# Performance work log

Hardware: AMD Instinct MI355X
Metric: run time of the kernel (lower is better)

Reference implementation:

```python
import jax, jax.numpy as jnp
import numpy as np

B, N, D, H = 2, 2048, 1024, 16
DH = D // H
SCALE = 1.0 / np.sqrt(DH).astype(np.float32)


def setup_inputs() -> dict:
    key = jax.random.key(0)
    k1, k2, k3, k4, k5 = jax.random.split(key, 5)
    x = jax.random.normal(k1, (B, N, D), dtype=jnp.float32)
    attn_bias = jax.random.normal(k2, (B, N, N), dtype=jnp.float32)
    # valid lengths in [N//2, N]; True = keep
    lengths = jax.random.randint(k3, (B,), N // 2, N + 1)
    key_padding_mask = jnp.arange(N)[None, :] < lengths[:, None]
    Wqkv = jax.random.normal(k4, (3 * D, D), dtype=jnp.float32) / np.sqrt(D)
    Wproj = jax.random.normal(k5, (D, D), dtype=jnp.float32) / np.sqrt(D)
    bproj = jnp.zeros((D,), dtype=jnp.float32)
    return {"x": x, "attn_bias": attn_bias, "key_padding_mask": key_padding_mask,
            "Wqkv": Wqkv, "Wproj": Wproj, "bproj": bproj}


def reference(x, attn_bias, key_padding_mask, Wqkv, Wproj, bproj):
    b, n, d = x.shape
    qkv = x @ Wqkv.T                                   # [B,N,3D]
    qkv = qkv.reshape(b, n, 3, H, DH)
    q = jnp.transpose(qkv[:, :, 0], (0, 2, 1, 3))      # [B,H,N,DH]
    k = jnp.transpose(qkv[:, :, 1], (0, 2, 1, 3))
    v = jnp.transpose(qkv[:, :, 2], (0, 2, 1, 3))
    attn = jnp.einsum('bhnd,bhmd->bhnm', q, k) * SCALE  # [B,H,N,N]
    attn = attn + attn_bias[:, None, :, :]
    attn = jnp.where(key_padding_mask[:, None, None, :], attn, -jnp.inf)
    attn = jax.nn.softmax(attn, axis=-1)
    y = jnp.einsum('bhnm,bhmd->bhnd', attn, v)          # [B,H,N,DH]
    y = jnp.transpose(y, (0, 2, 1, 3)).reshape(b, n, d)
    return y @ Wproj.T + bproj
```

## Files before the change

### kernel.cpp

```cpp
#include <hip/hip_runtime.h>
#include <hip/hip_bf16.h>

namespace {

typedef short short8 __attribute__((ext_vector_type(8)));
typedef float f32x4 __attribute__((ext_vector_type(4)));

#define L2E 1.4426950408889634f
#define SB() __builtin_amdgcn_sched_barrier(0)

__device__ __forceinline__ unsigned short f2bf(float f) {
  union { __hip_bfloat16 h; unsigned short u; } cv;
  cv.h = __float2bfloat16(f);
  return cv.u;
}

__device__ __forceinline__ unsigned cvt_pk_bf16(float lo, float hi) {
  unsigned r;
  asm("v_cvt_pk_bf16_f32 %0, %1, %2" : "=v"(r) : "v"(lo), "v"(hi));
  return r;
}

__device__ __forceinline__ void load_lds16(const void* g, void* l) {
  __builtin_amdgcn_global_load_lds((__attribute__((address_space(1))) void*)g,
                                   (__attribute__((address_space(3))) void*)l,
                                   16, 0, 0);
}

__device__ __forceinline__ int pi64(int rho) {
  const int c32 = rho & 32;
  const int o = (rho >> 4) & 1;
  const int g = (rho >> 2) & 3;
  const int s = rho & 3;
  return c32 + (o ? (((g ^ 2) << 3) + 4 + s) : ((g << 3) + s));
}

__global__ __launch_bounds__(256) void cvt_all(const float4* __restrict__ x,
                                               const float4* __restrict__ wqkv,
                                               const float4* __restrict__ wproj,
                                               const float4* __restrict__ biasf,
                                               ushort4* __restrict__ xb,
                                               ushort4* __restrict__ wqkvb,
                                               ushort4* __restrict__ wprojb,
                                               ushort4* __restrict__ bias16) {
  int i = blockIdx.x * 256 + threadIdx.x;
  if (i < 2097152) {
    const float4* src;
    ushort4* dst;
    int off;
    if (i < 1048576) { src = x; dst = xb; off = i; }
    else if (i < 1048576 + 786432) { src = wqkv; dst = wqkvb; off = i - 1048576; }
    else { src = wproj; dst = wprojb; off = i - (1048576 + 786432); }
    float4 f = src[off];
    ushort4 u;
    u.x = f2bf(f.x); u.y = f2bf(f.y); u.z = f2bf(f.z); u.w = f2bf(f.w);
    dst[off] = u;
  } else {
    const int off = i - 2097152;
    float4 f = biasf[off];
    ushort4 u;
    u.x = f2bf(f.x * L2E); u.y = f2bf(f.y * L2E);
    u.z = f2bf(f.z * L2E); u.w = f2bf(f.w * L2E);
    bias16[off] = u;
  }
}

__global__ __launch_bounds__(256) void gemm_qkv(const unsigned short* __restrict__ Xb,
                                                const unsigned short* __restrict__ Wb,
                                                unsigned short* __restrict__ qws,
                                                unsigned short* __restrict__ kws,
                                                unsigned short* __restrict__ vTws) {
  __shared__ unsigned short lA[128 * 32];
  __shared__ unsigned short lB[128 * 32];
  const int t = threadIdx.x;
  const int w = t >> 6, l = t & 63;
  const int wm = w >> 1, wn = w & 1;
  const int lr = l & 15, lg = l >> 4;
  const int row0 = blockIdx.x * 128, col0 = blockIdx.y * 128;
  const int srow = t >> 2;
  const int schunk = (t & 3) ^ (srow & 3);
  f32x4 acc[4][4] = {};
  for (int k0 = 0; k0 < 1024; k0 += 32) {
    __syncthreads();
    load_lds16(Xb + (size_t)(row0 + srow) * 1024 + k0 + schunk * 8, &lA[w * 512]);
    load_lds16(Xb + (size_t)(row0 + 64 + srow) * 1024 + k0 + schunk * 8, &lA[2048 + w * 512]);
    load_lds16(Wb + (size_t)(col0 + srow) * 1024 + k0 + schunk * 8, &lB[w * 512]);
    load_lds16(Wb + (size_t)(col0 + 64 + srow) * 1024 + k0 + schunk * 8, &lB[2048 + w * 512]);
    __syncthreads();
    short8 af[4], bf[4];
    const int rslot = (lg ^ (l & 3)) * 8;
#pragma unroll
    for (int mi = 0; mi < 4; ++mi)
      af[mi] = *(const short8*)&lA[(wm * 64 + mi * 16 + lr) * 32 + rslot];
#pragma unroll
    for (int ni = 0; ni < 4; ++ni)
      bf[ni] = *(const short8*)&lB[(wn * 64 + ni * 16 + lr) * 32 + rslot];
#pragma unroll
    for (int mi = 0; mi < 4; ++mi)
#pragma unroll
      for (int ni = 0; ni < 4; ++ni)
        acc[mi][ni] = __builtin_amdgcn_mfma_f32_16x16x32_bf16(af[mi], bf[ni], acc[mi][ni], 0, 0, 0);
  }
#pragma unroll
  for (int mi = 0; mi < 4; ++mi)
#pragma unroll
    for (int ni = 0; ni < 4; ++ni) {
      const int col = col0 + wn * 64 + ni * 16 + lr;
      const int s = col >> 10, rem = col & 1023;
      const int hh = rem >> 6, dh = rem & 63;
      const int row = row0 + wm * 64 + mi * 16 + lg * 4;
      const int bb = row >> 11, n = row & 2047;
      const size_t bh = (size_t)(bb * 16 + hh);
      if (s == 2) {
        ushort4 u4;
        u4.x = f2bf(acc[mi][ni][0]); u4.y = f2bf(acc[mi][ni][1]);
        u4.z = f2bf(acc[mi][ni][2]); u4.w = f2bf(acc[mi][ni][3]);
        *(ushort4*)&vTws[(bh * 64 + dh) * 2048 + n] = u4;
      } else if (s == 0) {
#pragma unroll
        for (int r = 0; r < 4; ++r)
          qws[(bh * 2048 + n + r) * 64 + dh] = f2bf(acc[mi][ni][r] * 0.18033688011112042f);
      } else {
#pragma unroll
        for (int r = 0; r < 4; ++r)
          kws[(bh * 2048 + n + r) * 64 + dh] = f2bf(acc[mi][ni][r]);
      }
    }
}

template <bool BB>
__global__ __launch_bounds__(256, 4) void attn_fwd(const unsigned short* __restrict__ qws,
                                                   const unsigned short* __restrict__ kws,
                                                   const unsigned short* __restrict__ vTws,
                                                   const float* __restrict__ bias,
                                                   const unsigned short* __restrict__ bias16,
                                                   const int* __restrict__ mask,
                                                   unsigned short* __restrict__ ctx) {
  __shared__ unsigned short lK[2][64 * 64];
  __shared__ unsigned short lVT[2][64 * 64];
  __shared__ int lred[4];
  const int t = threadIdx.x, w = t >> 6, l = t & 63;
  const int lr = l & 15, lg = l >> 4;
  const int xr7 = lr & 7;

  const int lin = blockIdx.x;
  const int xcd = lin & 7;
  const int r7 = lin >> 3;
  const int G = xcd * 8 + (r7 & 7);
  const int h = r7 >> 3;
  const int b = G & 1;
  const int qt = G >> 1;

  const size_t bh = (size_t)(b * 16 + h);
  const unsigned short* Q = qws + bh * (2048 * 64);
  const unsigned short* K = kws + bh * (2048 * 64);
  const unsigned short* VT = vTws + bh * (64 * 2048);

  const int* mrow = mask + b * 2048;
  int scnt = 0;
#pragma unroll
  for (int i = 0; i < 8; ++i) scnt += (mrow[t + i * 256] != 0);
#pragma unroll
  for (int d = 1; d < 64; d <<= 1) scnt += __shfl_xor(scnt, d, 64);
  if (l == 0) lred[w] = scnt;
  __syncthreads();
  const int len = lred[0] + lred[1] + lred[2] + lred[3];
  const int nt = ((((len + 63) >> 6) + 1) & ~1);

  const int qv = qt * 64 + w * 16 + lr;
  const short8 qf0 = *(const short8*)&Q[(size_t)qv * 64 + lg * 8];
  const short8 qf1 = *(const short8*)&Q[(size_t)qv * 64 + 32 + lg * 8];
  const float* bq = bias + (size_t)b * (2048 * 2048) + (size_t)qv * 2048;
  const unsigned short* bq16 = bias16 + (size_t)b * (2048 * 2048) + (size_t)qv * 2048;

  const int be = lg * 8, bo = ((lg ^ 2) * 8) + 4;
  const int boffs[4] = {be, bo, 32 + be, 32 + bo};

  short8 vones;
#pragma unroll
  for (int i = 0; i < 8; ++i) vones[i] = (short)0x3F80;

  f32x4 o[5] = {};

  const int sr = l >> 3;
  const int sc = ((l & 7) ^ sr) * 8;

  auto STAGE = [&](int ti2) {
    const int slot = ti2 & 1;
    const int kt2 = ti2 << 6;
#pragma unroll
    for (int u = 0; u < 2; ++u) {
      const int row = w * 16 + u * 8 + sr;
      load_lds16(K + (size_t)(kt2 + pi64(row)) * 64 + sc, &lK[slot][(w * 16 + u * 8) * 64]);
      load_lds16(VT + (size_t)row * 2048 + kt2 + sc, &lVT[slot][(w * 16 + u * 8) * 64]);
    }
  };
  auto LOADB = [&](auto& d, int ti2) {
    const int kt2 = ti2 << 6;
    if constexpr (BB) {
#pragma unroll
      for (int j = 0; j < 4; ++j) d[j] = *(const uint2*)&bq16[kt2 + boffs[j]];
    } else {
#pragma unroll
      for (int j = 0; j < 4; ++j) d[j] = *(const float4*)&bq[kt2 + boffs[j]];
    }
  };
  auto COMPUTE = [&](int ti, auto& b4, bool hn2) {
    const int slot = ti & 1;
    const int kt = ti << 6;
    const unsigned short* lKs = lK[slot];
    const unsigned short* lVs = lVT[slot];
    f32x4 s4[4];
    __builtin_amdgcn_s_setprio(1);
#pragma unroll
    for (int j = 0; j < 4; ++j) {
      f32x4 sj = {-16.f, -16.f, -16.f, -16.f};
      const int krow = (j * 16 + lr) * 64;
      short8 kf0 = *(const short8*)&lKs[krow + (lg ^ xr7) * 8];
      short8 kf1 = *(const short8*)&lKs[krow + ((lg + 4) ^ xr7) * 8];
      sj = __builtin_amdgcn_mfma_f32_16x16x32_bf16(kf0, qf0, sj, 0, 0, 0);
      sj = __builtin_amdgcn_mfma_f32_16x16x32_bf16(kf1, qf1, sj, 0, 0, 0);
      s4[j] = sj;
    }
    __builtin_amdgcn_s_setprio(0);
    if (kt + 64 <= len) {
#pragma unroll
      for (int j = 0; j < 4; ++j) {
        if constexpr (BB) {
          s4[j][0] += __uint_as_float(b4[j].x << 16);
          s4[j][1] += __uint_as_float(b4[j].x & 0xFFFF0000u);
          s4[j][2] += __uint_as_float(b4[j].y << 16);
          s4[j][3] += __uint_as_float(b4[j].y & 0xFFFF0000u);
        } else {
          s4[j][0] = fmaf(b4[j].x, L2E, s4[j][0]);
          s4[j][1] = fmaf(b4[j].y, L2E, s4[j][1]);
          s4[j][2] = fmaf(b4[j].z, L2E, s4[j][2]);
          s4[j][3] = fmaf(b4[j].w, L2E, s4[j][3]);
        }
      }
    } else {
#pragma unroll
      for (int j = 0; j < 4; ++j) {
        const int kb = kt + boffs[j];
        float bv[4];
        if constexpr (BB) {
          bv[0] = __uint_as_float(b4[j].x << 16);
          bv[1] = __uint_as_float(b4[j].x & 0xFFFF0000u);
          bv[2] = __uint_as_float(b4[j].y << 16);
          bv[3] = __uint_as_float(b4[j].y & 0xFFFF0000u);
#pragma unroll
          for (int r = 0; r < 4; ++r)
            s4[j][r] = (kb + r < len) ? (s4[j][r] + bv[r]) : -1e30f;
        } else {
          const float* bp = &b4[j].x;
#pragma unroll
          for (int r = 0; r < 4; ++r)
            s4[j][r] = (kb + r < len) ? fmaf(bp[r], L2E, s4[j][r]) : -1e30f;
        }
      }
    }
    if (hn2) LOADB(b4, ti + 2);
#pragma unroll
    for (int j = 0; j < 4; ++j)
#pragma unroll
      for (int r = 0; r < 4; ++r) s4[j][r] = __builtin_amdgcn_exp2f(s4[j][r]);
    unsigned wj0[4], wj1[4];
#pragma unroll
    for (int j = 0; j < 4; ++j) {
      wj0[j] = cvt_pk_bf16(s4[j][0], s4[j][1]);
      wj1[j] = cvt_pk_bf16(s4[j][2], s4[j][3]);
    }
#pragma unroll
    for (int c = 0; c < 2; ++c) {
      union { unsigned u[4]; short8 s8; } pu;
      pu.u[0] = wj0[2 * c];
      pu.u[1] = wj1[2 * c];
      pu.u[2] = (unsigned)__shfl_xor((int)wj0[2 * c + 1], 32, 64);
      pu.u[3] = (unsigned)__shfl_xor((int)wj1[2 * c + 1], 32, 64);
      __builtin_amdgcn_s_setprio(1);
#pragma unroll
      for (int ni = 0; ni < 4; ++ni) {
        short8 vf = *(const short8*)&lVs[(ni * 16 + lr) * 64 + ((c * 4 + lg) ^ xr7) * 8];
        o[ni] = __builtin_amdgcn_mfma_f32_16x16x32_bf16(pu.s8, vf, o[ni], 0, 0, 0);
      }
      o[4] = __builtin_amdgcn_mfma_f32_16x16x32_bf16(pu.s8, vones, o[4], 0, 0, 0);
      __builtin_amdgcn_s_setprio(0);
    }
  };

  float4 bA[4], bB[4];
  uint2 uA[4], uB[4];
  SB();
  STAGE(0);
  SB();
  if constexpr (BB) { LOADB(uA, 0); LOADB(uB, 1); }
  else              { LOADB(bA, 0); LOADB(bB, 1); }
  SB();
  asm volatile("s_waitcnt vmcnt(4)" ::: "memory");
  __builtin_amdgcn_s_barrier();
  SB();

  for (int ti = 0; ti < nt; ti += 2) {
    const bool h2 = (ti + 2 < nt);
    SB();
    STAGE(ti + 1);
    SB();
    if constexpr (BB) COMPUTE(ti, uA, h2); else COMPUTE(ti, bA, h2);
    SB();
    asm volatile("s_waitcnt vmcnt(4) lgkmcnt(0)" ::: "memory");
    __builtin_amdgcn_s_barrier();
    SB();
    if (h2) { STAGE(ti + 2); SB(); }
    if constexpr (BB) COMPUTE(ti + 1, uB, h2); else COMPUTE(ti + 1, bB, h2);
    if (h2) {
      SB();
      asm volatile("s_waitcnt vmcnt(4) lgkmcnt(0)" ::: "memory");
      __builtin_amdgcn_s_barrier();
      SB();
    }
  }

  float linv[4];
#pragma unroll
  for (int r = 0; r < 4; ++r) linv[r] = __builtin_amdgcn_rcpf(o[4][r]);
#pragma unroll
  for (int r = 0; r < 4; ++r) {
    const size_t orow = (size_t)b * 2048 + qt * 64 + w * 16 + lg * 4 + r;
#pragma unroll
    for (int ni = 0; ni < 4; ++ni)
      ctx[orow * 1024 + h * 64 + ni * 16 + lr] = f2bf(o[ni][r] * linv[r]);
  }
}

__global__ __launch_bounds__(256) void gemm_proj(const unsigned short* __restrict__ Cb,
                                                 const unsigned short* __restrict__ Wb,
                                                 const float* __restrict__ bproj,
                                                 float* __restrict__ out) {
  __shared__ unsigned short lA[128 * 32];
  __shared__ unsigned short lB[128 * 32];
  const int t = threadIdx.x;
  const int w = t >> 6, l = t & 63;
  const int wm = w >> 1, wn = w & 1;
  const int lr = l & 15, lg = l >> 4;
  const int row0 = blockIdx.x * 128, col0 = blockIdx.y * 128;
  const int srow = t >> 2;
  const int schunk = (t & 3) ^ (srow & 3);
  f32x4 acc[4][4] = {};
  for (int k0 = 0; k0 < 1024; k0 += 32) {
    __syncthreads();
    load_lds16(Cb + (size_t)(row0 + srow) * 1024 + k0 + schunk * 8, &lA[w * 512]);
    load_lds16(Cb + (size_t)(row0 + 64 + srow) * 1024 + k0 + schunk * 8, &lA[2048 + w * 512]);
    load_lds16(Wb + (size_t)(col0 + srow) * 1024 + k0 + schunk * 8, &lB[w * 512]);
    load_lds16(Wb + (size_t)(col0 + 64 + srow) * 1024 + k0 + schunk * 8, &lB[2048 + w * 512]);
    __syncthreads();
    short8 af[4], bf[4];
    const int rslot = (lg ^ (l & 3)) * 8;
#pragma unroll
    for (int mi = 0; mi < 4; ++mi)
      af[mi] = *(const short8*)&lA[(wm * 64 + mi * 16 + lr) * 32 + rslot];
#pragma unroll
    for (int ni = 0; ni < 4; ++ni)
      bf[ni] = *(const short8*)&lB[(wn * 64 + ni * 16 + lr) * 32 + rslot];
#pragma unroll
    for (int mi = 0; mi < 4; ++mi)
#pragma unroll
      for (int ni = 0; ni < 4; ++ni)
        acc[mi][ni] = __builtin_amdgcn_mfma_f32_16x16x32_bf16(af[mi], bf[ni], acc[mi][ni], 0, 0, 0);
  }
#pragma unroll
  for (int mi = 0; mi < 4; ++mi)
#pragma unroll
    for (int ni = 0; ni < 4; ++ni) {
      const int col = col0 + wn * 64 + ni * 16 + lr;
      const float bp = bproj[col];
#pragma unroll
      for (int r = 0; r < 4; ++r) {
        const int row = row0 + wm * 64 + mi * 16 + lg * 4 + r;
        out[(size_t)row * 1024 + col] = acc[mi][ni][r] + bp;
      }
    }
}

}

extern "C" void kernel_launch(void* const* d_in, const int* in_sizes, int n_in,
                              void* d_out, int out_size, void* d_ws, size_t ws_size,
                              hipStream_t stream) {
  (void)in_sizes; (void)n_in; (void)out_size;
  const float* x        = (const float*)d_in[0];
  const float* attnbias = (const float*)d_in[1];
  const int*   mask     = (const int*)d_in[2];
  const float* Wqkv     = (const float*)d_in[3];
  const float* Wproj    = (const float*)d_in[4];
  const float* bproj    = (const float*)d_in[5];
  float* out = (float*)d_out;

  unsigned short* ws     = (unsigned short*)d_ws;
  unsigned short* xb     = ws;
  unsigned short* wqkvb  = xb + 4194304;
  unsigned short* wprojb = wqkvb + 3145728;
  unsigned short* qws    = wprojb + 1048576;
  unsigned short* kws    = qws + 4194304;
  unsigned short* vTws   = kws + 4194304;
  unsigned short* ctxb   = vTws + 4194304;
  unsigned short* bias16 = ctxb + 4194304;

  const bool bb = ws_size >= (size_t)67108864;

  cvt_all<<<bb ? 16384 : 8192, 256, 0, stream>>>(
      (const float4*)x, (const float4*)Wqkv, (const float4*)Wproj,
      (const float4*)attnbias, (ushort4*)xb, (ushort4*)wqkvb, (ushort4*)wprojb,
      (ushort4*)bias16);
  gemm_qkv<<<dim3(32, 24), 256, 0, stream>>>(xb, wqkvb, qws, kws, vTws);
  if (bb)
    attn_fwd<true><<<1024, 256, 0, stream>>>(qws, kws, vTws, attnbias, bias16, mask, ctxb);
  else
    attn_fwd<false><<<1024, 256, 0, stream>>>(qws, kws, vTws, attnbias, bias16, mask, ctxb);
  gemm_proj<<<dim3(32, 8), 256, 0, stream>>>(ctxb, wprojb, bproj, out);
}
```

Baseline: 155.0 us.

## Overlap bias bf16 conversion with QKV GEMM and simplify mask length count

Moves the attention-bias fp32-to-bf16 conversion out of the standalone conversion kernel and into extra blocks of the QKV GEMM grid, so the memory-bound conversion runs alongside the compute-bound GEMM. In the attention kernel, each wave now counts the mask length on its own using int4 loads, which removes the shared-memory reduction and a block barrier. The trade-off is that the extra GEMM-grid blocks compete with GEMM tiles for compute units and bandwidth, and every wave repeats the mask reads.

```diff
diff --git a/kernel.cpp b/kernel.cpp
--- a/kernel.cpp
+++ b/kernel.cpp
@@ -38,41 +38,44 @@
 __global__ __launch_bounds__(256) void cvt_all(const float4* __restrict__ x,
                                                const float4* __restrict__ wqkv,
                                                const float4* __restrict__ wproj,
-                                               const float4* __restrict__ biasf,
                                                ushort4* __restrict__ xb,
                                                ushort4* __restrict__ wqkvb,
-                                               ushort4* __restrict__ wprojb,
-                                               ushort4* __restrict__ bias16) {
+                                               ushort4* __restrict__ wprojb) {
   int i = blockIdx.x * 256 + threadIdx.x;
-  if (i < 2097152) {
-    const float4* src;
-    ushort4* dst;
-    int off;
-    if (i < 1048576) { src = x; dst = xb; off = i; }
-    else if (i < 1048576 + 786432) { src = wqkv; dst = wqkvb; off = i - 1048576; }
-    else { src = wproj; dst = wprojb; off = i - (1048576 + 786432); }
-    float4 f = src[off];
-    ushort4 u;
-    u.x = f2bf(f.x); u.y = f2bf(f.y); u.z = f2bf(f.z); u.w = f2bf(f.w);
-    dst[off] = u;
-  } else {
-    const int off = i - 2097152;
-    float4 f = biasf[off];
-    ushort4 u;
-    u.x = f2bf(f.x * L2E); u.y = f2bf(f.y * L2E);
-    u.z = f2bf(f.z * L2E); u.w = f2bf(f.w * L2E);
-    bias16[off] = u;
-  }
+  const float4* src;
+  ushort4* dst;
+  int off;
+  if (i < 1048576) { src = x; dst = xb; off = i; }
+  else if (i < 1048576 + 786432) { src = wqkv; dst = wqkvb; off = i - 1048576; }
+  else { src = wproj; dst = wprojb; off = i - (1048576 + 786432); }
+  float4 f = src[off];
+  ushort4 u;
+  u.x = f2bf(f.x); u.y = f2bf(f.y); u.z = f2bf(f.z); u.w = f2bf(f.w);
+  dst[off] = u;
 }
 
 __global__ __launch_bounds__(256) void gemm_qkv(const unsigned short* __restrict__ Xb,
                                                 const unsigned short* __restrict__ Wb,
+                                                const float4* __restrict__ biasf,
+                                                ushort4* __restrict__ bias16,
                                                 unsigned short* __restrict__ qws,
                                                 unsigned short* __restrict__ kws,
                                                 unsigned short* __restrict__ vTws) {
   __shared__ unsigned short lA[128 * 32];
   __shared__ unsigned short lB[128 * 32];
   const int t = threadIdx.x;
+  if (blockIdx.x >= 32) {
+    const int nthr = 768 * 256;
+    int i = ((blockIdx.x - 32) + 32 * blockIdx.y) * 256 + t;
+    for (; i < 2097152; i += nthr) {
+      float4 f = biasf[i];
+      ushort4 u;
+      u.x = f2bf(f.x * L2E); u.y = f2bf(f.y * L2E);
+      u.z = f2bf(f.z * L2E); u.w = f2bf(f.w * L2E);
+      bias16[i] = u;
+    }
+    return;
+  }
   const int w = t >> 6, l = t & 63;
   const int wm = w >> 1, wn = w & 1;
   const int lr = l & 15, lg = l >> 4;
@@ -138,7 +141,6 @@
                                                    unsigned short* __restrict__ ctx) {
   __shared__ unsigned short lK[2][64 * 64];
   __shared__ unsigned short lVT[2][64 * 64];
-  __shared__ int lred[4];
   const int t = threadIdx.x, w = t >> 6, l = t & 63;
   const int lr = l & 15, lg = l >> 4;
   const int xr7 = lr & 7;
@@ -156,15 +158,16 @@
   const unsigned short* K = kws + bh * (2048 * 64);
   const unsigned short* VT = vTws + bh * (64 * 2048);
 
-  const int* mrow = mask + b * 2048;
+  const int4* m4 = (const int4*)(mask + b * 2048);
   int scnt = 0;
 #pragma unroll
-  for (int i = 0; i < 8; ++i) scnt += (mrow[t + i * 256] != 0);
+  for (int i = 0; i < 8; ++i) {
+    int4 v = m4[l + i * 64];
+    scnt += (v.x != 0) + (v.y != 0) + (v.z != 0) + (v.w != 0);
+  }
 #pragma unroll
   for (int d = 1; d < 64; d <<= 1) scnt += __shfl_xor(scnt, d, 64);
-  if (l == 0) lred[w] = scnt;
-  __syncthreads();
-  const int len = lred[0] + lred[1] + lred[2] + lred[3];
+  const int len = scnt;
   const int nt = ((((len + 63) >> 6) + 1) & ~1);
 
   const int qv = qt * 64 + w * 16 + lr;
@@ -407,11 +410,11 @@
 
   const bool bb = ws_size >= (size_t)67108864;
 
-  cvt_all<<<bb ? 16384 : 8192, 256, 0, stream>>>(
-      (const float4*)x, (const float4*)Wqkv, (const float4*)Wproj,
-      (const float4*)attnbias, (ushort4*)xb, (ushort4*)wqkvb, (ushort4*)wprojb,
-      (ushort4*)bias16);
-  gemm_qkv<<<dim3(32, 24), 256, 0, stream>>>(xb, wqkvb, qws, kws, vTws);
+  cvt_all<<<8192, 256, 0, stream>>>((const float4*)x, (const float4*)Wqkv,
+                                    (const float4*)Wproj, (ushort4*)xb,
+                                    (ushort4*)wqkvb, (ushort4*)wprojb);
+  gemm_qkv<<<dim3(bb ? 64 : 32, 24), 256, 0, stream>>>(
+      xb, wqkvb, (const float4*)attnbias, (ushort4*)bias16, qws, kws, vTws);
   if (bb)
     attn_fwd<true><<<1024, 256, 0, stream>>>(qws, kws, vTws, attnbias, bias16, mask, ctxb);
   else
```

Measured after the change: 162.4 us. +4.7%, slower.
